# Kernel tuning notes

Hardware: AMD Instinct MI355X
Metric: run time of the kernel (lower is better)

Reference implementation:

```python
import jax, jax.numpy as jnp
import numpy as np

N_ITER = 4  # matches init_kwargs n_iter
N, K, D = 32768, 32, 32


def setup_inputs() -> dict:
    key = jax.random.key(0)
    k1, k2 = jax.random.split(key)
    data = jax.random.normal(k1, (N, D), dtype=jnp.float32)
    # torch init: means ~ randn, covariances = stacked identity, weights uniform
    means = jax.random.normal(k2, (K, D), dtype=jnp.float32)
    covariances = jnp.tile(jnp.eye(D, dtype=jnp.float32)[None], (K, 1, 1))
    weights = jnp.ones((K,), dtype=jnp.float32) / K
    return {"data": data, "means": means, "covariances": covariances, "weights": weights}


def _em(data, means, covariances, weights, n_iter):
    for _ in range(n_iter):
        # ---- E-step (vectorized over components, replacing the python loop) ----
        inv = jnp.linalg.inv(covariances)          # [K,D,D]
        det = jnp.linalg.det(covariances)          # [K]
        diff = data[:, None, :] - means[None]      # [N,K,D]
        # quadratic form diff^T Sigma^{-1} diff per point/component
        q = jnp.einsum('nkd,kde,nke->nk', diff, inv, diff)  # [N,K]
        probs = weights[None, :] * jnp.exp(-0.5 * q) / jnp.sqrt(det)[None, :]
        probs = probs / probs.sum(axis=1, keepdims=True)    # responsibilities [N,K]
        # ---- M-step (torch updates weights first; cov uses diff w.r.t. OLD means) ----
        weights = probs.mean(axis=0)                         # [K]
        Nk = probs.sum(axis=0)                               # [K]
        means = (probs.T @ data) / Nk[:, None]               # [K,D] (new means)
        covariances = jnp.einsum('nk,nkd,nke->kde', probs, diff, diff) / Nk[:, None, None]
    return means, covariances, weights


def reference(data, means, covariances, weights):
    return _em(data, means, covariances, weights, N_ITER)
```

## Files before the change

kernel.cpp:

```cpp
#include <hip/hip_runtime.h>

#define NPTS 32768
#define PREC 1057

__global__ __launch_bounds__(256) void prep_kernel(
    const float* __restrict__ cov, const float* __restrict__ means_in,
    const float* __restrict__ wts,
    float* __restrict__ A2, float* __restrict__ b2,
    float* __restrict__ cvec, float* __restrict__ coef)
{
    int k   = blockIdx.x;
    int tid = threadIdx.x;
    __shared__ float M[32][66];
    __shared__ float mu[32];
    __shared__ float bb[32];

    for (int i = tid; i < 1024; i += 256) {
        int r = i >> 5, c = i & 31;
        M[r][c]      = cov[k * 1024 + i];
        M[r][32 + c] = (r == c) ? 1.0f : 0.0f;
    }
    if (tid < 32) mu[tid] = means_in[k * 32 + tid];
    __syncthreads();

    int r  = tid >> 3;
    int c0 = (tid & 7) * 8;
    float det = 1.0f;
    for (int s = 0; s < 32; ++s) {
        float piv = M[s][s];
        det *= piv;
        float rp = 1.0f / piv;
        float f  = (r != s) ? M[r][s] : 0.0f;
        __syncthreads();
        if (tid < 64) M[s][tid] *= rp;
        __syncthreads();
        if (r != s) {
            #pragma unroll
            for (int j = 0; j < 8; ++j) M[r][c0 + j] -= f * M[s][c0 + j];
        }
        __syncthreads();
    }

    for (int i = tid; i < 1024; i += 256) {
        int d = i >> 5, e = i & 31;
        A2[(i >> 1) * 64 + k * 2 + (i & 1)] = M[d][32 + e];
    }
    if (tid < 32) {
        int d = tid;
        float bd = 0.0f;
        #pragma unroll
        for (int e = 0; e < 32; ++e) bd += M[d][32 + e] * mu[e];
        bb[d] = bd;
        b2[(d >> 1) * 64 + k * 2 + (d & 1)] = bd;
    }
    __syncthreads();
    if (tid == 0) {
        float cc = 0.0f;
        #pragma unroll
        for (int d = 0; d < 32; ++d) cc += mu[d] * bb[d];
        cvec[k] = cc;
        coef[k] = wts[k] / sqrtf(det);
    }
}

__global__ __launch_bounds__(512, 2) void estep_kernel(
    const float* __restrict__ data, const float* __restrict__ A2g,
    const float* __restrict__ b2g, const float* __restrict__ cvec,
    const float* __restrict__ coefg, float* __restrict__ P)
{
    __shared__ alignas(16) float A2s[32768];
    int tid = threadIdx.x;
    for (int i = tid; i < 8192; i += 512)
        ((float4*)A2s)[i] = ((const float4*)A2g)[i];
    __syncthreads();

    int lane = tid & 63;
    int wv   = tid >> 6;
    int k    = lane & 31;
    int g    = lane >> 5;
    int p0   = blockIdx.x * 64 + wv * 8 + g * 4;

    float x0[32], x1[32], x2[32], x3[32];
    {
        const float4* dp0 = (const float4*)(data + (size_t)p0 * 32);
        const float4* dp1 = (const float4*)(data + (size_t)(p0 + 1) * 32);
        const float4* dp2 = (const float4*)(data + (size_t)(p0 + 2) * 32);
        const float4* dp3 = (const float4*)(data + (size_t)(p0 + 3) * 32);
        #pragma unroll
        for (int j = 0; j < 8; ++j) {
            float4 v0 = dp0[j]; x0[4*j]=v0.x; x0[4*j+1]=v0.y; x0[4*j+2]=v0.z; x0[4*j+3]=v0.w;
            float4 v1 = dp1[j]; x1[4*j]=v1.x; x1[4*j+1]=v1.y; x1[4*j+2]=v1.z; x1[4*j+3]=v1.w;
            float4 v2 = dp2[j]; x2[4*j]=v2.x; x2[4*j+1]=v2.y; x2[4*j+2]=v2.z; x2[4*j+3]=v2.w;
            float4 v3 = dp3[j]; x3[4*j]=v3.x; x3[4*j+1]=v3.y; x3[4*j+2]=v3.z; x3[4*j+3]=v3.w;
        }
    }

    float q0 = 0.0f, q1 = 0.0f, q2 = 0.0f, q3 = 0.0f;
    #pragma unroll
    for (int d = 0; d < 32; ++d) {
        float r0=0, s0=0, r1=0, s1=0, r2=0, s2=0, r3=0, s3=0;
        #pragma unroll
        for (int c = 0; c < 16; ++c) {
            float2 a = *(const float2*)&A2s[(d * 16 + c) * 64 + (k << 1)];
            r0 += a.x * x0[2*c];  s0 += a.y * x0[2*c+1];
            r1 += a.x * x1[2*c];  s1 += a.y * x1[2*c+1];
            r2 += a.x * x2[2*c];  s2 += a.y * x2[2*c+1];
            r3 += a.x * x3[2*c];  s3 += a.y * x3[2*c+1];
        }
        q0 += x0[d] * (r0 + s0);
        q1 += x1[d] * (r1 + s1);
        q2 += x2[d] * (r2 + s2);
        q3 += x3[d] * (r3 + s3);
    }

    float b0=0, b1=0, b2v=0, b3=0;
    #pragma unroll
    for (int d2 = 0; d2 < 16; ++d2) {
        float2 b = *(const float2*)&b2g[d2 * 64 + (k << 1)];
        b0 += b.x * x0[2*d2] + b.y * x0[2*d2+1];
        b1 += b.x * x1[2*d2] + b.y * x1[2*d2+1];
        b2v+= b.x * x2[2*d2] + b.y * x2[2*d2+1];
        b3 += b.x * x3[2*d2] + b.y * x3[2*d2+1];
    }
    float cc = cvec[k], cf = coefg[k];
    float e0 = cf * __expf(-0.5f * (q0 - 2.0f * b0  + cc));
    float e1 = cf * __expf(-0.5f * (q1 - 2.0f * b1  + cc));
    float e2 = cf * __expf(-0.5f * (q2 - 2.0f * b2v + cc));
    float e3 = cf * __expf(-0.5f * (q3 - 2.0f * b3  + cc));

    float t0=e0, t1=e1, t2=e2, t3=e3;
    #pragma unroll
    for (int m = 16; m >= 1; m >>= 1) {
        t0 += __shfl_xor(t0, m, 64);
        t1 += __shfl_xor(t1, m, 64);
        t2 += __shfl_xor(t2, m, 64);
        t3 += __shfl_xor(t3, m, 64);
    }
    P[(size_t)p0 * 32 + k]       = e0 / t0;
    P[(size_t)(p0 + 1) * 32 + k] = e1 / t1;
    P[(size_t)(p0 + 2) * 32 + k] = e2 / t2;
    P[(size_t)(p0 + 3) * 32 + k] = e3 / t3;
}

__global__ __launch_bounds__(256, 4) void mstep_kernel(
    const float* __restrict__ data, const float* __restrict__ P,
    float* __restrict__ partial)
{
    int k     = blockIdx.x & 31;
    int chunk = blockIdx.x >> 5;
    int tid   = threadIdx.x;
    int tile  = tid & 31;
    int ng    = tid >> 5;
    int dt    = tile >> 2;
    int et    = tile & 3;

    __shared__ alignas(16) float SH[8 * 1088];

    float acc[4][8];
    #pragma unroll
    for (int i = 0; i < 4; ++i)
        #pragma unroll
        for (int j = 0; j < 8; ++j) acc[i][j] = 0.0f;
    float m0=0, m1=0, m2=0, m3=0, nk=0;

    int base = chunk * 1024;
    for (int stage = 0; stage < 4; ++stage) {
        __syncthreads();
        for (int i = tid; i < 2048; i += 256)
            ((float4*)SH)[i] = ((const float4*)(data + (size_t)(base + stage * 256) * 32))[i];
        __syncthreads();
        const float4* X4 = (const float4*)SH;
        int nb = ng * 32;
        #pragma unroll 4
        for (int nn = 0; nn < 32; ++nn) {
            int n  = nb + nn;
            float p = P[(size_t)(base + stage * 256 + n) * 32 + k];
            float4 xd  = X4[n * 8 + dt];
            float4 xe0 = X4[n * 8 + et * 2];
            float4 xe1 = X4[n * 8 + et * 2 + 1];
            float p0 = p * xd.x, p1 = p * xd.y, p2 = p * xd.z, p3 = p * xd.w;
            acc[0][0]+=p0*xe0.x; acc[0][1]+=p0*xe0.y; acc[0][2]+=p0*xe0.z; acc[0][3]+=p0*xe0.w;
            acc[0][4]+=p0*xe1.x; acc[0][5]+=p0*xe1.y; acc[0][6]+=p0*xe1.z; acc[0][7]+=p0*xe1.w;
            acc[1][0]+=p1*xe0.x; acc[1][1]+=p1*xe0.y; acc[1][2]+=p1*xe0.z; acc[1][3]+=p1*xe0.w;
            acc[1][4]+=p1*xe1.x; acc[1][5]+=p1*xe1.y; acc[1][6]+=p1*xe1.z; acc[1][7]+=p1*xe1.w;
            acc[2][0]+=p2*xe0.x; acc[2][1]+=p2*xe0.y; acc[2][2]+=p2*xe0.z; acc[2][3]+=p2*xe0.w;
            acc[2][4]+=p2*xe1.x; acc[2][5]+=p2*xe1.y; acc[2][6]+=p2*xe1.z; acc[2][7]+=p2*xe1.w;
            acc[3][0]+=p3*xe0.x; acc[3][1]+=p3*xe0.y; acc[3][2]+=p3*xe0.z; acc[3][3]+=p3*xe0.w;
            acc[3][4]+=p3*xe1.x; acc[3][5]+=p3*xe1.y; acc[3][6]+=p3*xe1.z; acc[3][7]+=p3*xe1.w;
            if (et == 0) { m0 += p0; m1 += p1; m2 += p2; m3 += p3; }
            if (tile == 0) nk += p;
        }
    }
    __syncthreads();

    {
        float* Sg = SH + ng * 1088;
        #pragma unroll
        for (int i = 0; i < 4; ++i) {
            int row = dt * 4 + i;
            #pragma unroll
            for (int j = 0; j < 8; ++j) {
                int col = (et * 8 + j + dt) & 31;
                Sg[row * 32 + col] = acc[i][j];
            }
        }
        if (et == 0) {
            Sg[1024 + dt * 4 + 0] = m0; Sg[1024 + dt * 4 + 1] = m1;
            Sg[1024 + dt * 4 + 2] = m2; Sg[1024 + dt * 4 + 3] = m3;
        }
        if (tile == 0) Sg[1056] = nk;
    }
    __syncthreads();

    float* out = partial + (size_t)(chunk * 32 + k) * PREC;
    for (int e = tid; e < PREC; e += 256) {
        int ridx;
        if (e < 1024) {
            int row = e >> 5, col = e & 31;
            ridx = row * 32 + ((col + (row >> 2)) & 31);
        } else ridx = e;
        float s = 0.0f;
        #pragma unroll
        for (int gg = 0; gg < 8; ++gg) s += SH[gg * 1088 + ridx];
        out[e] = s;
    }
}

__global__ __launch_bounds__(256) void finalize_kernel(
    const float* __restrict__ partial, const float* __restrict__ means_old,
    float* __restrict__ covS, float* __restrict__ means_new_ws,
    float* __restrict__ wS, float* __restrict__ out)
{
    int k = blockIdx.x, tid = threadIdx.x;
    __shared__ float SS[PREC];
    __shared__ float MU[32];
    __shared__ float MB[32];

    for (int e = tid; e < PREC; e += 256) {
        float s = 0.0f;
        for (int ch = 0; ch < 32; ++ch)
            s += partial[(size_t)(ch * 32 + k) * PREC + e];
        SS[e] = s;
    }
    if (tid < 32) MU[tid] = means_old[k * 32 + tid];
    __syncthreads();

    float nk = SS[1056];
    float rnk = 1.0f / nk;
    if (tid < 32) {
        float mb = SS[1024 + tid] * rnk;
        MB[tid] = mb;
        means_new_ws[k * 32 + tid] = mb;
        out[k * 32 + tid] = mb;
    }
    __syncthreads();

    for (int idx = tid; idx < 1024; idx += 256) {
        int d = idx >> 5, e = idx & 31;
        float c = SS[idx] * rnk - MU[d] * MB[e] - MB[d] * MU[e] + MU[d] * MU[e];
        covS[k * 1024 + idx] = c;
        out[1024 + k * 1024 + idx] = c;
    }
    if (tid == 0) {
        float w = nk * (1.0f / (float)NPTS);
        wS[k] = w;
        out[33792 + k] = w;
    }
}

extern "C" void kernel_launch(void* const* d_in, const int* in_sizes, int n_in,
                              void* d_out, int out_size, void* d_ws, size_t ws_size,
                              hipStream_t stream) {
    (void)in_sizes; (void)n_in; (void)out_size; (void)ws_size;
    const float* data   = (const float*)d_in[0];
    const float* means0 = (const float*)d_in[1];
    const float* cov0   = (const float*)d_in[2];
    const float* w0     = (const float*)d_in[3];

    float* ws      = (float*)d_ws;
    float* A2      = ws + 0;
    float* b2      = ws + 32768;
    float* cvec    = ws + 33792;
    float* coef    = ws + 33824;
    float* meansA  = ws + 33856;
    float* meansB  = ws + 34880;
    float* covS    = ws + 35904;
    float* wS      = ws + 68672;
    float* P       = ws + 68704;
    float* partial = ws + 1117280;

    float* mi = meansA;
    float* mo = meansB;
    for (int it = 0; it < 4; ++it) {
        const float* cov_src = (it == 0) ? cov0   : covS;
        const float* mns_src = (it == 0) ? means0 : mi;
        const float* w_src   = (it == 0) ? w0     : wS;
        prep_kernel<<<32, 256, 0, stream>>>(cov_src, mns_src, w_src, A2, b2, cvec, coef);
        estep_kernel<<<512, 512, 0, stream>>>(data, A2, b2, cvec, coef, P);
        mstep_kernel<<<1024, 256, 0, stream>>>(data, P, partial);
        finalize_kernel<<<32, 256, 0, stream>>>(partial, mns_src, covS, mo, wS, (float*)d_out);
        float* tmp = mi; mi = mo; mo = tmp;
    }
}
```

Before: 500.1 us.

## Exploit covariance symmetry in E-step, fuse prep into finalize, stage P in LDS

The E-step quadratic form now reads only the upper triangle of the symmetric inverse covariance plus its diagonal, which shrinks the LDS table from 128KB to about 76KB. With that smaller table the kernel processes two points per thread instead of four and raises occupancy, with 1024 blocks. The inverse/pack prep is merged into the finalize kernel, removing one launch per iteration, and constants are packed into one contiguous buffer loaded into LDS. The M-step stages each block's P column in shared memory with a single coalesced-ish load, and remaps block indices so blocks with the same k run together. Risks include rounding differences from the 2q-diag reformulation and a serial while loop in the packing code.

```diff
diff --git a/kernel.cpp b/kernel.cpp
--- a/kernel.cpp
+++ b/kernel.cpp
@@ -2,37 +2,21 @@
 
 #define NPTS 32768
 #define PREC 1057
-
-__global__ __launch_bounds__(256) void prep_kernel(
-    const float* __restrict__ cov, const float* __restrict__ means_in,
-    const float* __restrict__ wts,
-    float* __restrict__ A2, float* __restrict__ b2,
-    float* __restrict__ cvec, float* __restrict__ coef)
-{
-    int k   = blockIdx.x;
-    int tid = threadIdx.x;
-    __shared__ float M[32][66];
-    __shared__ float mu[32];
-    __shared__ float bb[32];
-
-    for (int i = tid; i < 1024; i += 256) {
-        int r = i >> 5, c = i & 31;
-        M[r][c]      = cov[k * 1024 + i];
-        M[r][32 + c] = (r == c) ? 1.0f : 0.0f;
-    }
-    if (tid < 32) mu[tid] = means_in[k * 32 + tid];
-    __syncthreads();
-
+#define ELDSF 19520
+
+__device__ __forceinline__ void invert_pack(float M[32][66], const float* mu, float wk,
+    int k, int tid, float* A2t, float* DG, float* b2, float* cvec, float* coef, float* bb)
+{
     int r  = tid >> 3;
     int c0 = (tid & 7) * 8;
     float det = 1.0f;
     for (int s = 0; s < 32; ++s) {
         float piv = M[s][s];
         det *= piv;
-        float rp = 1.0f / piv;
-        float f  = (r != s) ? M[r][s] : 0.0f;
-        __syncthreads();
-        if (tid < 64) M[s][tid] *= rp;
+        float rpv = 1.0f / piv;
+        float f   = (r != s) ? M[r][s] : 0.0f;
+        __syncthreads();
+        if (tid < 64) M[s][tid] *= rpv;
         __syncthreads();
         if (r != s) {
             #pragma unroll
@@ -40,18 +24,24 @@
         }
         __syncthreads();
     }
-
-    for (int i = tid; i < 1024; i += 256) {
-        int d = i >> 5, e = i & 31;
-        A2[(i >> 1) * 64 + k * 2 + (i & 1)] = M[d][32 + e];
+    for (int t = tid; t < 272; t += 256) {
+        int d = 0, b = 0;
+        while (t >= b + ((33 - d) >> 1)) { b += (33 - d) >> 1; ++d; }
+        int j  = t - b;
+        int e0 = d + 2 * j, e1 = e0 + 1;
+        A2t[t * 64 + k * 2 + 0] = M[d][32 + e0];
+        A2t[t * 64 + k * 2 + 1] = (e1 < 32) ? M[d][32 + e1] : 0.0f;
+    }
+    if (tid < 16) {
+        DG[tid * 64 + k * 2 + 0] = M[2 * tid][32 + 2 * tid];
+        DG[tid * 64 + k * 2 + 1] = M[2 * tid + 1][32 + 2 * tid + 1];
     }
     if (tid < 32) {
-        int d = tid;
         float bd = 0.0f;
         #pragma unroll
-        for (int e = 0; e < 32; ++e) bd += M[d][32 + e] * mu[e];
-        bb[d] = bd;
-        b2[(d >> 1) * 64 + k * 2 + (d & 1)] = bd;
+        for (int e = 0; e < 32; ++e) bd += M[tid][32 + e] * mu[e];
+        bb[tid] = bd;
+        b2[(tid >> 1) * 64 + k * 2 + (tid & 1)] = bd;
     }
     __syncthreads();
     if (tid == 0) {
@@ -59,18 +49,36 @@
         #pragma unroll
         for (int d = 0; d < 32; ++d) cc += mu[d] * bb[d];
         cvec[k] = cc;
-        coef[k] = wts[k] / sqrtf(det);
-    }
-}
-
-__global__ __launch_bounds__(512, 2) void estep_kernel(
+        coef[k] = wk / sqrtf(det);
+    }
+}
+
+__global__ __launch_bounds__(256) void prep0_kernel(
+    const float* __restrict__ cov0, const float* __restrict__ means0,
+    const float* __restrict__ w0,
+    float* __restrict__ A2t, float* __restrict__ DG, float* __restrict__ b2,
+    float* __restrict__ cvec, float* __restrict__ coef)
+{
+    int k = blockIdx.x, tid = threadIdx.x;
+    __shared__ float M[32][66];
+    __shared__ float MU[32], BB[32];
+    for (int i = tid; i < 1024; i += 256) {
+        int r = i >> 5, c = i & 31;
+        M[r][c]      = cov0[k * 1024 + i];
+        M[r][32 + c] = (r == c) ? 1.0f : 0.0f;
+    }
+    if (tid < 32) MU[tid] = means0[k * 32 + tid];
+    __syncthreads();
+    invert_pack(M, MU, w0[k], k, tid, A2t, DG, b2, cvec, coef, BB);
+}
+
+__global__ __launch_bounds__(512, 4) void estep_kernel(
     const float* __restrict__ data, const float* __restrict__ A2g,
-    const float* __restrict__ b2g, const float* __restrict__ cvec,
-    const float* __restrict__ coefg, float* __restrict__ P)
-{
-    __shared__ alignas(16) float A2s[32768];
+    float* __restrict__ P)
+{
+    __shared__ alignas(16) float A2s[ELDSF];
     int tid = threadIdx.x;
-    for (int i = tid; i < 8192; i += 512)
+    for (int i = tid; i < ELDSF / 4; i += 512)
         ((float4*)A2s)[i] = ((const float4*)A2g)[i];
     __syncthreads();
 
@@ -78,83 +86,82 @@
     int wv   = tid >> 6;
     int k    = lane & 31;
     int g    = lane >> 5;
-    int p0   = blockIdx.x * 64 + wv * 8 + g * 4;
-
-    float x0[32], x1[32], x2[32], x3[32];
+    int p0   = blockIdx.x * 32 + wv * 4 + g * 2;
+
+    float x0[32], x1[32];
     {
         const float4* dp0 = (const float4*)(data + (size_t)p0 * 32);
         const float4* dp1 = (const float4*)(data + (size_t)(p0 + 1) * 32);
-        const float4* dp2 = (const float4*)(data + (size_t)(p0 + 2) * 32);
-        const float4* dp3 = (const float4*)(data + (size_t)(p0 + 3) * 32);
         #pragma unroll
         for (int j = 0; j < 8; ++j) {
-            float4 v0 = dp0[j]; x0[4*j]=v0.x; x0[4*j+1]=v0.y; x0[4*j+2]=v0.z; x0[4*j+3]=v0.w;
-            float4 v1 = dp1[j]; x1[4*j]=v1.x; x1[4*j+1]=v1.y; x1[4*j+2]=v1.z; x1[4*j+3]=v1.w;
-            float4 v2 = dp2[j]; x2[4*j]=v2.x; x2[4*j+1]=v2.y; x2[4*j+2]=v2.z; x2[4*j+3]=v2.w;
-            float4 v3 = dp3[j]; x3[4*j]=v3.x; x3[4*j+1]=v3.y; x3[4*j+2]=v3.z; x3[4*j+3]=v3.w;
-        }
-    }
-
-    float q0 = 0.0f, q1 = 0.0f, q2 = 0.0f, q3 = 0.0f;
+            float4 v = dp0[j]; x0[4*j]=v.x; x0[4*j+1]=v.y; x0[4*j+2]=v.z; x0[4*j+3]=v.w;
+            float4 u = dp1[j]; x1[4*j]=u.x; x1[4*j+1]=u.y; x1[4*j+2]=u.z; x1[4*j+3]=u.w;
+        }
+    }
+
+    float q0 = 0.0f, q1 = 0.0f;
+    int t = 0;
     #pragma unroll
     for (int d = 0; d < 32; ++d) {
-        float r0=0, s0=0, r1=0, s1=0, r2=0, s2=0, r3=0, s3=0;
-        #pragma unroll
-        for (int c = 0; c < 16; ++c) {
-            float2 a = *(const float2*)&A2s[(d * 16 + c) * 64 + (k << 1)];
-            r0 += a.x * x0[2*c];  s0 += a.y * x0[2*c+1];
-            r1 += a.x * x1[2*c];  s1 += a.y * x1[2*c+1];
-            r2 += a.x * x2[2*c];  s2 += a.y * x2[2*c+1];
-            r3 += a.x * x3[2*c];  s3 += a.y * x3[2*c+1];
-        }
-        q0 += x0[d] * (r0 + s0);
-        q1 += x1[d] * (r1 + s1);
-        q2 += x2[d] * (r2 + s2);
-        q3 += x3[d] * (r3 + s3);
-    }
-
-    float b0=0, b1=0, b2v=0, b3=0;
-    #pragma unroll
-    for (int d2 = 0; d2 < 16; ++d2) {
-        float2 b = *(const float2*)&b2g[d2 * 64 + (k << 1)];
-        b0 += b.x * x0[2*d2] + b.y * x0[2*d2+1];
-        b1 += b.x * x1[2*d2] + b.y * x1[2*d2+1];
-        b2v+= b.x * x2[2*d2] + b.y * x2[2*d2+1];
-        b3 += b.x * x3[2*d2] + b.y * x3[2*d2+1];
-    }
-    float cc = cvec[k], cf = coefg[k];
-    float e0 = cf * __expf(-0.5f * (q0 - 2.0f * b0  + cc));
-    float e1 = cf * __expf(-0.5f * (q1 - 2.0f * b1  + cc));
-    float e2 = cf * __expf(-0.5f * (q2 - 2.0f * b2v + cc));
-    float e3 = cf * __expf(-0.5f * (q3 - 2.0f * b3  + cc));
-
-    float t0=e0, t1=e1, t2=e2, t3=e3;
+        const int np = (33 - d) >> 1;
+        float w0 = 0.0f, w1 = 0.0f;
+        #pragma unroll
+        for (int j = 0; j < np; ++j) {
+            const int e0 = d + 2 * j;
+            const int e1 = (e0 + 1 < 32) ? e0 + 1 : 31;
+            float2 a = *(const float2*)&A2s[(t + j) * 64 + (k << 1)];
+            w0 = __builtin_fmaf(a.y, x0[e1], __builtin_fmaf(a.x, x0[e0], w0));
+            w1 = __builtin_fmaf(a.y, x1[e1], __builtin_fmaf(a.x, x1[e0], w1));
+        }
+        t += np;
+        q0 += x0[d] * w0;
+        q1 += x1[d] * w1;
+    }
+    float d20 = 0.0f, d21 = 0.0f;
+    #pragma unroll
+    for (int i = 0; i < 16; ++i) {
+        float2 a = *(const float2*)&A2s[17408 + i * 64 + (k << 1)];
+        float ta = a.x * x0[2*i];     d20 = __builtin_fmaf(ta, x0[2*i],   d20);
+        float tb = a.y * x0[2*i+1];   d20 = __builtin_fmaf(tb, x0[2*i+1], d20);
+        float tc = a.x * x1[2*i];     d21 = __builtin_fmaf(tc, x1[2*i],   d21);
+        float td = a.y * x1[2*i+1];   d21 = __builtin_fmaf(td, x1[2*i+1], d21);
+    }
+    float bx0 = 0.0f, bx1 = 0.0f;
+    #pragma unroll
+    for (int i = 0; i < 16; ++i) {
+        float2 b = *(const float2*)&A2s[18432 + i * 64 + (k << 1)];
+        bx0 += b.x * x0[2*i] + b.y * x0[2*i+1];
+        bx1 += b.x * x1[2*i] + b.y * x1[2*i+1];
+    }
+    float cc = A2s[19456 + k], cf = A2s[19488 + k];
+    float e0v = cf * __expf(-0.5f * ((2.0f * q0 - d20) - 2.0f * bx0 + cc));
+    float e1v = cf * __expf(-0.5f * ((2.0f * q1 - d21) - 2.0f * bx1 + cc));
+
+    float t0 = e0v, t1 = e1v;
     #pragma unroll
     for (int m = 16; m >= 1; m >>= 1) {
         t0 += __shfl_xor(t0, m, 64);
         t1 += __shfl_xor(t1, m, 64);
-        t2 += __shfl_xor(t2, m, 64);
-        t3 += __shfl_xor(t3, m, 64);
-    }
-    P[(size_t)p0 * 32 + k]       = e0 / t0;
-    P[(size_t)(p0 + 1) * 32 + k] = e1 / t1;
-    P[(size_t)(p0 + 2) * 32 + k] = e2 / t2;
-    P[(size_t)(p0 + 3) * 32 + k] = e3 / t3;
+    }
+    P[(size_t)p0 * 32 + k]       = e0v / t0;
+    P[(size_t)(p0 + 1) * 32 + k] = e1v / t1;
 }
 
 __global__ __launch_bounds__(256, 4) void mstep_kernel(
     const float* __restrict__ data, const float* __restrict__ P,
     float* __restrict__ partial)
 {
-    int k     = blockIdx.x & 31;
-    int chunk = blockIdx.x >> 5;
+    int bid   = blockIdx.x;
+    int k     = bid >> 5;
+    int chunk = (bid & 7) * 4 + ((bid >> 3) & 3);
     int tid   = threadIdx.x;
     int tile  = tid & 31;
     int ng    = tid >> 5;
     int dt    = tile >> 2;
     int et    = tile & 3;
 
-    __shared__ alignas(16) float SH[8 * 1088];
+    __shared__ alignas(16) float SH[9216];
+    float* ps = SH + 8192;
 
     float acc[4][8];
     #pragma unroll
@@ -168,13 +175,14 @@
         __syncthreads();
         for (int i = tid; i < 2048; i += 256)
             ((float4*)SH)[i] = ((const float4*)(data + (size_t)(base + stage * 256) * 32))[i];
+        ps[tid] = P[(size_t)(base + stage * 256 + tid) * 32 + k];
         __syncthreads();
         const float4* X4 = (const float4*)SH;
         int nb = ng * 32;
         #pragma unroll 4
         for (int nn = 0; nn < 32; ++nn) {
-            int n  = nb + nn;
-            float p = P[(size_t)(base + stage * 256 + n) * 32 + k];
+            int n   = nb + nn;
+            float p = ps[n];
             float4 xd  = X4[n * 8 + dt];
             float4 xe0 = X4[n * 8 + et * 2];
             float4 xe1 = X4[n * 8 + et * 2 + 1];
@@ -226,15 +234,16 @@
     }
 }
 
-__global__ __launch_bounds__(256) void finalize_kernel(
-    const float* __restrict__ partial, const float* __restrict__ means_old,
-    float* __restrict__ covS, float* __restrict__ means_new_ws,
-    float* __restrict__ wS, float* __restrict__ out)
+__global__ __launch_bounds__(256) void finprep_kernel(
+    const float* __restrict__ partial, const float* __restrict__ means_old, int do_prep,
+    float* __restrict__ A2t, float* __restrict__ DG, float* __restrict__ b2,
+    float* __restrict__ cvec, float* __restrict__ coef,
+    float* __restrict__ means_new, float* __restrict__ out)
 {
     int k = blockIdx.x, tid = threadIdx.x;
     __shared__ float SS[PREC];
-    __shared__ float MU[32];
-    __shared__ float MB[32];
+    __shared__ float MU[32], MB[32], BB[32];
+    __shared__ float M[32][66];
 
     for (int e = tid; e < PREC; e += 256) {
         float s = 0.0f;
@@ -245,26 +254,29 @@
     if (tid < 32) MU[tid] = means_old[k * 32 + tid];
     __syncthreads();
 
-    float nk = SS[1056];
+    float nk  = SS[1056];
     float rnk = 1.0f / nk;
+    float wk  = nk * (1.0f / (float)NPTS);
     if (tid < 32) {
         float mb = SS[1024 + tid] * rnk;
         MB[tid] = mb;
-        means_new_ws[k * 32 + tid] = mb;
+        means_new[k * 32 + tid] = mb;
         out[k * 32 + tid] = mb;
     }
+    if (tid == 0) out[33792 + k] = wk;
     __syncthreads();
 
     for (int idx = tid; idx < 1024; idx += 256) {
         int d = idx >> 5, e = idx & 31;
         float c = SS[idx] * rnk - MU[d] * MB[e] - MB[d] * MU[e] + MU[d] * MU[e];
-        covS[k * 1024 + idx] = c;
         out[1024 + k * 1024 + idx] = c;
-    }
-    if (tid == 0) {
-        float w = nk * (1.0f / (float)NPTS);
-        wS[k] = w;
-        out[33792 + k] = w;
+        M[d][e]      = c;
+        M[d][32 + e] = (d == e) ? 1.0f : 0.0f;
+    }
+    __syncthreads();
+
+    if (do_prep) {
+        invert_pack(M, MB, wk, k, tid, A2t, DG, b2, cvec, coef, BB);
     }
 }
 
@@ -278,27 +290,24 @@
     const float* w0     = (const float*)d_in[3];
 
     float* ws      = (float*)d_ws;
-    float* A2      = ws + 0;
-    float* b2      = ws + 32768;
-    float* cvec    = ws + 33792;
-    float* coef    = ws + 33824;
-    float* meansA  = ws + 33856;
-    float* meansB  = ws + 34880;
-    float* covS    = ws + 35904;
-    float* wS      = ws + 68672;
-    float* P       = ws + 68704;
-    float* partial = ws + 1117280;
-
-    float* mi = meansA;
-    float* mo = meansB;
+    float* A2t     = ws + 0;
+    float* DG      = ws + 17408;
+    float* b2      = ws + 18432;
+    float* cvec    = ws + 19456;
+    float* coef    = ws + 19488;
+    float* meansA  = ws + 19520;
+    float* meansB  = ws + 20544;
+    float* P       = ws + 21568;
+    float* partial = ws + 1070144;
+
+    prep0_kernel<<<32, 256, 0, stream>>>(cov0, means0, w0, A2t, DG, b2, cvec, coef);
+    const float* mold = means0;
     for (int it = 0; it < 4; ++it) {
-        const float* cov_src = (it == 0) ? cov0   : covS;
-        const float* mns_src = (it == 0) ? means0 : mi;
-        const float* w_src   = (it == 0) ? w0     : wS;
-        prep_kernel<<<32, 256, 0, stream>>>(cov_src, mns_src, w_src, A2, b2, cvec, coef);
-        estep_kernel<<<512, 512, 0, stream>>>(data, A2, b2, cvec, coef, P);
+        float* mnew = (it & 1) ? meansB : meansA;
+        estep_kernel<<<1024, 512, 0, stream>>>(data, ws, P);
         mstep_kernel<<<1024, 256, 0, stream>>>(data, P, partial);
-        finalize_kernel<<<32, 256, 0, stream>>>(partial, mns_src, covS, mo, wS, (float*)d_out);
-        float* tmp = mi; mi = mo; mo = tmp;
-    }
-}
+        finprep_kernel<<<32, 256, 0, stream>>>(partial, mold, (it < 3) ? 1 : 0,
+                                               A2t, DG, b2, cvec, coef, mnew, (float*)d_out);
+        mold = mnew;
+    }
+}
```

Measured after the change: 509.8 us. About the same (+1.9%).
